# Kernel optimization log

Hardware: AMD Instinct MI355X
Metric: run time of the kernel (lower is better)

The kernel has to match this reference:

```python
import jax, jax.numpy as jnp
import numpy as np

NX = 32; NY = 32; D = 2; K = 5; SCALE = 1.0
DX = 2.0 * SCALE / (NX - 1)
N = NX * NY

def _region_kernel():
    # kernel_size^d grid of offsets with spacing DX, centered at 0
    t = (jnp.arange(K, dtype=jnp.float32) - (K - 1) / 2.0) * DX
    gx, gy = jnp.meshgrid(t, t, indexing='ij')
    return jnp.stack((gx, gy), -1).reshape(-1, D)  # (K*K, 2)

def _build_cov(scaling, transform):
    # lower-triangular L: diag = scaling, strict lower = transform; cov = L L^T
    L = jnp.zeros((scaling.shape[0], D, D), scaling.dtype)
    L = L.at[:, 0, 0].set(scaling[:, 0])
    L = L.at[:, 1, 1].set(scaling[:, 1])
    L = L.at[:, 1, 0].set(transform[:, 0])
    return L @ jnp.swapaxes(L, -1, -2)

def reference(means, u, scaling, transform, conv_w, conv_b, emb_w, emb_b,
              lin1_w, lin1_b, sol_w, sol_b, tr_w, tr_b, sc_w, sc_b, tf_w, tf_b):
    cov = _build_cov(scaling, transform)          # (N,2,2)
    conics = jnp.linalg.inv(cov)                  # (N,2,2)
    # local sample gather: every Gaussian contributes K*K sample points
    samples = (means[:, None, :] + _region_kernel()[None]).reshape(-1, D)  # (S,2)
    # global Gaussian mixture evaluation at all sample points (no_grad in torch)
    diff = samples[:, None, :] - means[None, :, :]            # (S,N,2)
    Cd = jnp.einsum('nde,sne->snd', conics, diff)             # (S,N,2)
    G = jnp.exp(-0.5 * jnp.einsum('snd,snd->sn', diff, Cd))   # (S,N) densities
    w = G * u[None, :, 0]                                     # (S,N)
    u_s = jnp.sum(w, -1, keepdims=True)                       # (S,1)
    # Hessian of mixture: sum_j w_j ((C_j d)(C_j d)^T - C_j)
    wc = w[..., None] * Cd
    uxx = jnp.einsum('snd,sne->sde', wc, Cd) - jnp.einsum('sn,nde->sde', w, conics)
    pde = (uxx[:, 0, 0] + uxx[:, 1, 1])[:, None]              # diffusion rhs = laplacian
    mask = jnp.all(jnp.abs(samples) < SCALE, -1)[:, None].astype(u.dtype)
    img = jnp.concatenate((u_s, pde, mask), -1)               # (S, 3)
    img = img.reshape(N, K * K, 3).transpose(0, 2, 1).reshape(N, 3, K, K)
    img = jax.lax.stop_gradient(img)  # torch computes samples under no_grad
    params = jnp.concatenate((means, u, scaling, transform), -1)  # (N,6)
    # 4 stacked Networks (solution, translation, scale, transform); conv kernel
    # spans the whole K x K patch so Conv2d reduces to a tensordot
    y = jnp.tanh(jnp.einsum('ichw,mochw->mio', img, conv_w) + conv_b[:, None, :])
    e = jnp.tanh(jnp.einsum('ip,mpq->miq', params, emb_w) + emb_b[:, None, :])
    h = jnp.concatenate((y, e), -1)                               # (4,N,80)
    h = jnp.tanh(jnp.einsum('mio,moq->miq', h, lin1_w) + lin1_b[:, None, :])
    u_new = u + (h[0] @ sol_w + sol_b)
    means_new = means + (h[1] @ tr_w + tr_b)
    scaling_new = scaling * jnp.exp(h[2] @ sc_w + sc_b)
    transform_new = transform + (h[3] @ tf_w + tf_b)
    return jnp.concatenate((u_new, means_new, scaling_new, transform_new), -1)  # (N,6)

def setup_inputs() -> dict:
    key = jax.random.key(0)
    ks = jax.random.split(key, 14)
    tx = jnp.linspace(-1.0, 1.0, NX, dtype=jnp.float32) * SCALE
    ty = jnp.linspace(-1.0, 1.0, NY, dtype=jnp.float32) * SCALE
    gx, gy = jnp.meshgrid(tx, ty, indexing='ij')
    means = jnp.stack((gx, gy), -1).reshape(-1, D)
    scaling = jnp.full((N, D), float(np.exp(-4.5)) * SCALE, dtype=jnp.float32)
    transform = jnp.zeros((N, 1), jnp.float32)
    # initial u: gaussian bump (as in the torch __init__ default branch)
    u = jnp.exp(-0.5 * (means ** 2).sum(-1) / (0.1 * SCALE))[:, None].astype(jnp.float32)
    def p(k, shape, s):
        return jax.random.normal(k, shape, jnp.float32) * s
    return {
        'means': means, 'u': u, 'scaling': scaling, 'transform': transform,
        'conv_w': p(ks[0], (4, 50, 3, K, K), 0.08), 'conv_b': p(ks[1], (4, 50), 0.02),
        'emb_w': p(ks[2], (4, 6, 30), 0.3), 'emb_b': p(ks[3], (4, 30), 0.02),
        'lin1_w': p(ks[4], (4, 80, 80), 0.1), 'lin1_b': p(ks[5], (4, 80), 0.02),
        'sol_w': p(ks[6], (80, 1), 0.1), 'sol_b': jnp.zeros((1,), jnp.float32),
        'tr_w': p(ks[7], (80, 2), 0.1), 'tr_b': jnp.zeros((2,), jnp.float32),
        'sc_w': p(ks[8], (80, 2), 0.1), 'sc_b': jnp.zeros((2,), jnp.float32),
        'tf_w': p(ks[9], (80, 1), 0.1), 'tf_b': jnp.zeros((1,), jnp.float32),
    }
```

## Files before the change

### kernel.cpp

```cpp
#include <hip/hip_runtime.h>
#include <math.h>


namespace {

constexpr int NG = 1024;
constexpr int K2 = 25;
constexpr float DXF = 2.0f / 31.0f;
constexpr float NHALF_LOG2E = -0.72134752044448170367f;
constexpr float TWO_LOG2E   = 2.88539008177792681472f;
constexpr float LOG2E       = 1.44269504088896340736f;

__device__ __forceinline__ float fast_tanh(float x) {
  x = fminf(9.0f, fmaxf(-9.0f, x));
  float t = __builtin_amdgcn_exp2f(TWO_LOG2E * x);
  return (t - 1.0f) * __builtin_amdgcn_rcpf(t + 1.0f);
}

__global__ __launch_bounds__(256) void k_prep(
    const float* __restrict__ conv_w, float* __restrict__ cwT)
{
  int idx = blockIdx.x * 256 + threadIdx.x;
  if (idx < 4 * 75 * 50) {
    int m = idx / 3750, r = idx - m * 3750;
    int c = r / 50, o = r - c * 50;
    cwT[idx] = conv_w[(m * 50 + o) * 75 + c];
  }
}

__global__ __launch_bounds__(256) void k_mixture(
    const float* __restrict__ means, const float* __restrict__ uu,
    const float* __restrict__ scaling, const float* __restrict__ transform,
    float* __restrict__ img )
{
  __shared__ float4 gp[NG];
  __shared__ float2 gq[NG];
  __shared__ float r_us[4][64];
  __shared__ float r_pde[4][64];

  const int tid = threadIdx.x;

  for (int g = tid; g < NG; g += 256) {
    float mx = means[2 * g], my = means[2 * g + 1];
    float s0 = scaling[2 * g], s1 = scaling[2 * g + 1];
    float t0 = transform[g];
    float c  = 1.0f / (s1 * s1);
    float is0 = 1.0f / s0;
    float b  = -t0 * c * is0;
    float a  = (t0 * t0 * c + 1.0f) * is0 * is0;
    gp[g] = make_float4(mx, my, a, b);
    gq[g] = make_float2(c, uu[g]);
  }
  __syncthreads();

  const int sub  = tid >> 6;
  const int lane = tid & 63;
  const int s  = blockIdx.x * 64 + lane;
  const int i  = s / K2;
  const int k  = s - i * K2;
  const int kx = k / 5;
  const int ky = k - kx * 5;
  const float sx = means[2 * i]     + (float)(kx - 2) * DXF;
  const float sy = means[2 * i + 1] + (float)(ky - 2) * DXF;

  float us = 0.0f, pde = 0.0f;
  const int g0 = sub * 256;
#pragma unroll 4
  for (int j = 0; j < 256; ++j) {
    const int g = g0 + j;
    float4 p  = gp[g];
    float2 qv = gq[g];
    float dx = sx - p.x, dy = sy - p.y;
    float a = p.z, b = p.w, c = qv.x;
    float Cd0 = a * dx + b * dy;
    float Cd1 = b * dx + c * dy;
    float q   = dx * Cd0 + dy * Cd1;
    float w   = qv.y * __builtin_amdgcn_exp2f(NHALF_LOG2E * q);
    us  += w;
    pde += w * (Cd0 * Cd0 + Cd1 * Cd1 - (a + c));
  }
  r_us[sub][lane]  = us;
  r_pde[sub][lane] = pde;
  __syncthreads();

  if (tid < 64) {
    float U = r_us[0][tid] + r_us[1][tid] + r_us[2][tid] + r_us[3][tid];
    float P = r_pde[0][tid] + r_pde[1][tid] + r_pde[2][tid] + r_pde[3][tid];
    float mask = (fabsf(sx) < 1.0f && fabsf(sy) < 1.0f) ? 1.0f : 0.0f;
    img[i * 75 + k]      = U;
    img[i * 75 + 25 + k] = P;
    img[i * 75 + 50 + k] = mask;
  }
}

__global__ __launch_bounds__(256) void k_net(
    const float* __restrict__ img,
    const float* __restrict__ means, const float* __restrict__ uu,
    const float* __restrict__ scaling, const float* __restrict__ transform,
    const float* __restrict__ cwT, const float* __restrict__ conv_b,
    const float* __restrict__ emb_w, const float* __restrict__ emb_b,
    const float* __restrict__ lin1_w, const float* __restrict__ lin1_b,
    const float* __restrict__ sol_w, const float* __restrict__ sol_b,
    const float* __restrict__ tr_w, const float* __restrict__ tr_b,
    const float* __restrict__ sc_w, const float* __restrict__ sc_b,
    const float* __restrict__ tf_w, const float* __restrict__ tf_b,
    float* __restrict__ out)
{
  const int i = blockIdx.x;
  const int tid = threadIdx.x;

  __shared__ float simg[75];
  __shared__ float sparams[6];
  __shared__ float h[320];
  __shared__ float h2[320];
  __shared__ float hpart[6][8];

  if (tid < 75) simg[tid] = img[i * 75 + tid];
  if (tid < 6) {
    float v;
    if (tid < 2)       v = means[2 * i + tid];
    else if (tid == 2) v = uu[i];
    else if (tid < 5)  v = scaling[2 * i + (tid - 3)];
    else               v = transform[i];
    sparams[tid] = v;
  }
  __syncthreads();

  if (tid < 200) {
    const int m = tid / 50, o = tid - m * 50;
    const float* w = cwT + m * 3750 + o;
    float acc = conv_b[m * 50 + o];
#pragma unroll
    for (int c = 0; c < 75; ++c) acc = fmaf(simg[c], w[c * 50], acc);
    h[m * 80 + o] = fast_tanh(acc);
  }
  if (tid >= 200) {
    for (int e = tid - 200; e < 120; e += 56) {
      const int m = e / 30, q = e - m * 30;
      float acc = emb_b[m * 30 + q];
#pragma unroll
      for (int p = 0; p < 6; ++p) acc = fmaf(sparams[p], emb_w[(m * 6 + p) * 30 + q], acc);
      h[m * 80 + 50 + q] = fast_tanh(acc);
    }
  }
  __syncthreads();

  for (int idx = tid; idx < 320; idx += 256) {
    const int m = idx / 80, q = idx - m * 80;
    const float* lw = lin1_w + m * 6400 + q;
    const float* hh = h + m * 80;
    float acc = lin1_b[m * 80 + q];
#pragma unroll 8
    for (int j = 0; j < 80; ++j) acc = fmaf(hh[j], lw[j * 80], acc);
    h2[idx] = fast_tanh(acc);
  }
  __syncthreads();

  if (tid < 48) {
    const int o = tid >> 3, c8 = tid & 7;
    const int m = (o == 0) ? 0 : (o < 3) ? 1 : (o < 5) ? 2 : 3;
    const float* wp; int stride;
    if (o == 0)      { wp = sol_w;            stride = 1; }
    else if (o < 3)  { wp = tr_w + (o - 1);   stride = 2; }
    else if (o < 5)  { wp = sc_w + (o - 3);   stride = 2; }
    else             { wp = tf_w;             stride = 1; }
    const float* hh = h2 + m * 80;
    float acc = 0.0f;
    const int j0 = c8 * 10;
#pragma unroll
    for (int j = 0; j < 10; ++j) acc = fmaf(hh[j0 + j], wp[(j0 + j) * stride], acc);
    hpart[o][c8] = acc;
  }
  __syncthreads();

  if (tid < 6) {
    float acc = 0.0f;
#pragma unroll
    for (int c = 0; c < 8; ++c) acc += hpart[tid][c];
    float res;
    if (tid == 0)      res = sparams[2] + acc + sol_b[0];
    else if (tid < 3)  res = sparams[tid - 1] + acc + tr_b[tid - 1];
    else if (tid < 5)  res = sparams[tid] * __builtin_amdgcn_exp2f(LOG2E * (acc + sc_b[tid - 3]));
    else               res = sparams[5] + acc + tf_b[0];
    out[i * 6 + tid] = res;
  }
}

}

extern "C" void kernel_launch(void* const* d_in, const int* in_sizes, int n_in,
                              void* d_out, int out_size, void* d_ws, size_t ws_size,
                              hipStream_t stream) {
  const float* means     = (const float*)d_in[0];
  const float* uu        = (const float*)d_in[1];
  const float* scaling   = (const float*)d_in[2];
  const float* transform = (const float*)d_in[3];
  const float* conv_w    = (const float*)d_in[4];
  const float* conv_b    = (const float*)d_in[5];
  const float* emb_w     = (const float*)d_in[6];
  const float* emb_b     = (const float*)d_in[7];
  const float* lin1_w    = (const float*)d_in[8];
  const float* lin1_b    = (const float*)d_in[9];
  const float* sol_w     = (const float*)d_in[10];
  const float* sol_b     = (const float*)d_in[11];
  const float* tr_w      = (const float*)d_in[12];
  const float* tr_b      = (const float*)d_in[13];
  const float* sc_w      = (const float*)d_in[14];
  const float* sc_b      = (const float*)d_in[15];
  const float* tf_w      = (const float*)d_in[16];
  const float* tf_b      = (const float*)d_in[17];

  float* cwT = (float*)d_ws;
  float* img = (float*)d_ws + 16384;
  float* out = (float*)d_out;

  k_prep<<<59, 256, 0, stream>>>(conv_w, cwT);
  k_mixture<<<400, 256, 0, stream>>>(means, uu, scaling, transform, img);
  k_net<<<1024, 256, 0, stream>>>(img, means, uu, scaling, transform,
                                  cwT, conv_b, emb_w, emb_b, lin1_w, lin1_b,
                                  sol_w, sol_b, tr_w, tr_b, sc_w, sc_b, tf_w, tf_b,
                                  out);
}
```

Baseline: 121.7 us.

## Fuse Gaussian mixture evaluation into per-Gaussian network kernel

Merges the mixture-evaluation kernel into the network kernel so each block computes its own 25 sample densities and Laplacians in shared memory before running the MLP. This removes one kernel launch and the global round trip of the intermediate image buffer. In exchange, every block now recomputes all 1024 Gaussian conic parameters into LDS, and the larger LDS footprint may reduce occupancy.

```diff
diff --git a/kernel.cpp b/kernel.cpp
--- a/kernel.cpp
+++ b/kernel.cpp
@@ -5,7 +5,6 @@
 namespace {
 
 constexpr int NG = 1024;
-constexpr int K2 = 25;
 constexpr float DXF = 2.0f / 31.0f;
 constexpr float NHALF_LOG2E = -0.72134752044448170367f;
 constexpr float TWO_LOG2E   = 2.88539008177792681472f;
@@ -28,73 +27,7 @@
   }
 }
 
-__global__ __launch_bounds__(256) void k_mixture(
-    const float* __restrict__ means, const float* __restrict__ uu,
-    const float* __restrict__ scaling, const float* __restrict__ transform,
-    float* __restrict__ img )
-{
-  __shared__ float4 gp[NG];
-  __shared__ float2 gq[NG];
-  __shared__ float r_us[4][64];
-  __shared__ float r_pde[4][64];
-
-  const int tid = threadIdx.x;
-
-  for (int g = tid; g < NG; g += 256) {
-    float mx = means[2 * g], my = means[2 * g + 1];
-    float s0 = scaling[2 * g], s1 = scaling[2 * g + 1];
-    float t0 = transform[g];
-    float c  = 1.0f / (s1 * s1);
-    float is0 = 1.0f / s0;
-    float b  = -t0 * c * is0;
-    float a  = (t0 * t0 * c + 1.0f) * is0 * is0;
-    gp[g] = make_float4(mx, my, a, b);
-    gq[g] = make_float2(c, uu[g]);
-  }
-  __syncthreads();
-
-  const int sub  = tid >> 6;
-  const int lane = tid & 63;
-  const int s  = blockIdx.x * 64 + lane;
-  const int i  = s / K2;
-  const int k  = s - i * K2;
-  const int kx = k / 5;
-  const int ky = k - kx * 5;
-  const float sx = means[2 * i]     + (float)(kx - 2) * DXF;
-  const float sy = means[2 * i + 1] + (float)(ky - 2) * DXF;
-
-  float us = 0.0f, pde = 0.0f;
-  const int g0 = sub * 256;
-#pragma unroll 4
-  for (int j = 0; j < 256; ++j) {
-    const int g = g0 + j;
-    float4 p  = gp[g];
-    float2 qv = gq[g];
-    float dx = sx - p.x, dy = sy - p.y;
-    float a = p.z, b = p.w, c = qv.x;
-    float Cd0 = a * dx + b * dy;
-    float Cd1 = b * dx + c * dy;
-    float q   = dx * Cd0 + dy * Cd1;
-    float w   = qv.y * __builtin_amdgcn_exp2f(NHALF_LOG2E * q);
-    us  += w;
-    pde += w * (Cd0 * Cd0 + Cd1 * Cd1 - (a + c));
-  }
-  r_us[sub][lane]  = us;
-  r_pde[sub][lane] = pde;
-  __syncthreads();
-
-  if (tid < 64) {
-    float U = r_us[0][tid] + r_us[1][tid] + r_us[2][tid] + r_us[3][tid];
-    float P = r_pde[0][tid] + r_pde[1][tid] + r_pde[2][tid] + r_pde[3][tid];
-    float mask = (fabsf(sx) < 1.0f && fabsf(sy) < 1.0f) ? 1.0f : 0.0f;
-    img[i * 75 + k]      = U;
-    img[i * 75 + 25 + k] = P;
-    img[i * 75 + 50 + k] = mask;
-  }
-}
-
-__global__ __launch_bounds__(256) void k_net(
-    const float* __restrict__ img,
+__global__ __launch_bounds__(256) void k_fused(
     const float* __restrict__ means, const float* __restrict__ uu,
     const float* __restrict__ scaling, const float* __restrict__ transform,
     const float* __restrict__ cwT, const float* __restrict__ conv_b,
@@ -106,16 +39,30 @@
     const float* __restrict__ tf_w, const float* __restrict__ tf_b,
     float* __restrict__ out)
 {
-  const int i = blockIdx.x;
-  const int tid = threadIdx.x;
-
+  __shared__ float4 gp[NG];
+  __shared__ float2 gq[NG];
+  __shared__ float r_us[10][25];
+  __shared__ float r_pde[10][25];
   __shared__ float simg[75];
   __shared__ float sparams[6];
   __shared__ float h[320];
   __shared__ float h2[320];
   __shared__ float hpart[6][8];
 
-  if (tid < 75) simg[tid] = img[i * 75 + tid];
+  const int i = blockIdx.x;
+  const int tid = threadIdx.x;
+
+  for (int g = tid; g < NG; g += 256) {
+    float mx = means[2 * g], my = means[2 * g + 1];
+    float s0 = scaling[2 * g], s1 = scaling[2 * g + 1];
+    float t0 = transform[g];
+    float cc  = 1.0f / (s1 * s1);
+    float is0 = 1.0f / s0;
+    float bb  = -t0 * cc * is0;
+    float aa  = (t0 * t0 * cc + 1.0f) * is0 * is0;
+    gp[g] = make_float4(mx, my, aa, bb);
+    gq[g] = make_float2(cc, uu[g]);
+  }
   if (tid < 6) {
     float v;
     if (tid < 2)       v = means[2 * i + tid];
@@ -123,6 +70,47 @@
     else if (tid < 5)  v = scaling[2 * i + (tid - 3)];
     else               v = transform[i];
     sparams[tid] = v;
+  }
+  __syncthreads();
+
+  if (tid < 250) {
+    const int c = tid / 25;
+    const int s = tid - c * 25;
+    const int kx = s / 5, ky = s - kx * 5;
+    const float sx = means[2 * i]     + (float)(kx - 2) * DXF;
+    const float sy = means[2 * i + 1] + (float)(ky - 2) * DXF;
+    const int base = (c < 4) ? 103 * c : 412 + 102 * (c - 4);
+    const int len  = (c < 4) ? 103 : 102;
+    float us = 0.0f, pde = 0.0f;
+#pragma unroll 4
+    for (int j = 0; j < len; ++j) {
+      const int g = base + j;
+      float4 p  = gp[g];
+      float2 qv = gq[g];
+      float dx = sx - p.x, dy = sy - p.y;
+      float a = p.z, b = p.w, cc = qv.x;
+      float Cd0 = a * dx + b * dy;
+      float Cd1 = b * dx + cc * dy;
+      float q   = dx * Cd0 + dy * Cd1;
+      float w   = qv.y * __builtin_amdgcn_exp2f(NHALF_LOG2E * q);
+      us  += w;
+      pde += w * (Cd0 * Cd0 + Cd1 * Cd1 - (a + cc));
+    }
+    r_us[c][s]  = us;
+    r_pde[c][s] = pde;
+  }
+  __syncthreads();
+
+  if (tid < 25) {
+    float U = 0.0f, P = 0.0f;
+#pragma unroll
+    for (int c = 0; c < 10; ++c) { U += r_us[c][tid]; P += r_pde[c][tid]; }
+    const int kx = tid / 5, ky = tid - kx * 5;
+    const float sx = sparams[0] + (float)(kx - 2) * DXF;
+    const float sy = sparams[1] + (float)(ky - 2) * DXF;
+    simg[tid]      = U;
+    simg[25 + tid] = P;
+    simg[50 + tid] = (fabsf(sx) < 1.0f && fabsf(sy) < 1.0f) ? 1.0f : 0.0f;
   }
   __syncthreads();
 
@@ -211,13 +199,11 @@
   const float* tf_b      = (const float*)d_in[17];
 
   float* cwT = (float*)d_ws;
-  float* img = (float*)d_ws + 16384;
   float* out = (float*)d_out;
 
   k_prep<<<59, 256, 0, stream>>>(conv_w, cwT);
-  k_mixture<<<400, 256, 0, stream>>>(means, uu, scaling, transform, img);
-  k_net<<<1024, 256, 0, stream>>>(img, means, uu, scaling, transform,
-                                  cwT, conv_b, emb_w, emb_b, lin1_w, lin1_b,
-                                  sol_w, sol_b, tr_w, tr_b, sc_w, sc_b, tf_w, tf_b,
-                                  out);
-}
+  k_fused<<<1024, 256, 0, stream>>>(means, uu, scaling, transform,
+                                    cwT, conv_b, emb_w, emb_b, lin1_w, lin1_b,
+                                    sol_w, sol_b, tr_w, tr_b, sc_w, sc_b, tf_w, tf_b,
+                                    out);
+}
```

Result: faster. 111.9 us (-8.1%).
